# Optimization experiments

Measured on AMD Instinct MI355X. Metric: run time of the kernel, lower is better.

## Reference

```python
import jax, jax.numpy as jnp
import numpy as np

N_NODES, N_FEAT, HIDDEN, N_CLASSES, N_EDGES = 100000, 64, 64, 16, 1600000


def setup_inputs() -> dict:
    key = jax.random.key(0)
    ks = jax.random.split(key, 10)
    x = jax.random.normal(ks[0], (N_NODES, N_FEAT), dtype=jnp.float32)
    edge_index = jax.random.randint(ks[1], (2, N_EDGES), 0, N_NODES, dtype=jnp.int32)
    edge_weight = jax.random.uniform(ks[2], (N_EDGES,), dtype=jnp.float32)
    # Glorot-style init for GCNConv weights, zero bias (as in torch_geometric)
    W1 = jax.random.normal(ks[3], (N_FEAT, HIDDEN), dtype=jnp.float32) / np.float32(np.sqrt(N_FEAT))
    b1 = jnp.zeros((HIDDEN,), jnp.float32)
    W2 = jax.random.normal(ks[4], (HIDDEN, HIDDEN), dtype=jnp.float32) / np.float32(np.sqrt(HIDDEN))
    b2 = jnp.zeros((HIDDEN,), jnp.float32)
    W3 = jax.random.normal(ks[5], (HIDDEN, N_CLASSES), dtype=jnp.float32) / np.float32(np.sqrt(HIDDEN))
    b3 = jnp.zeros((N_CLASSES,), jnp.float32)
    return {"x": x, "edge_index": edge_index, "edge_weight": edge_weight,
            "W1": W1, "b1": b1, "W2": W2, "b2": b2, "W3": W3, "b3": b3}


def _gcn_norm(edge_index, edge_weight, num_nodes):
    """Add self-loops (weight 1) and compute symmetric D^-1/2 A D^-1/2 norm."""
    loop = jnp.arange(num_nodes, dtype=edge_index.dtype)
    src = jnp.concatenate([edge_index[0], loop])
    dst = jnp.concatenate([edge_index[1], loop])
    ew = jnp.concatenate([edge_weight, jnp.ones((num_nodes,), edge_weight.dtype)])
    deg = jax.ops.segment_sum(ew, dst, num_segments=num_nodes)
    dis = jnp.where(deg > 0, jax.lax.rsqrt(jnp.where(deg > 0, deg, 1.0)), 0.0)
    norm = dis[src] * ew * dis[dst]  # [E+N]
    return src, dst, norm


def reference(x, edge_index, edge_weight, W1, b1, W2, b2, W3, b3):
    N = x.shape[0]
    src, dst, norm = _gcn_norm(edge_index, edge_weight, N)

    def conv(h, W, b):
        hw = h @ W                                   # [N, out]
        msg = norm[:, None] * hw[src]                # [E+N, out]
        return jax.ops.segment_sum(msg, dst, num_segments=N) + b

    # conv1 + ReLU (dropout is identity in eval mode)
    h = jax.nn.relu(conv(x, W1, b1))
    # one hidden GCNConv layer (num_layer=3)
    h = jax.nn.relu(conv(h, W2, b2))
    logits = conv(h, W3, b3)                         # [N, C]
    out = jax.nn.log_softmax(logits, axis=1)
    return (out, logits, logits)
```

## Files before the change

kernel.cpp:

```cpp
#include <hip/hip_runtime.h>
#include <hip/hip_bf16.h>

#define N_FEAT 64
#define NBW 9
#define SRC_BITS 23
#define CAP 9216

typedef unsigned short u16;
typedef __attribute__((ext_vector_type(8))) short short8;
typedef __attribute__((ext_vector_type(4))) float f32x4;

__device__ inline u16 f2bf(float f) {
    unsigned u = __float_as_uint(f);
    u += 0x7fffu + ((u >> 16) & 1u);
    return (u16)(u >> 16);
}


__device__ inline void packW(const float* __restrict__ W, uint4* __restrict__ Wpk,
                             int ncb, int wcols, int tid) {
    int nf = ncb * 2 * 64;
    for (int f = tid; f < nf; f += 256) {
        int cb = f >> 7;
        int s  = (f >> 6) & 1;
        int lane = f & 63;
        int kb = lane >> 4, c16 = lane & 15;
        union { uint4 q; u16 u[8]; } pk;
        #pragma unroll
        for (int i = 0; i < 8; ++i) {
            int k = s * 32 + kb * 8 + i;
            pk.u[i] = f2bf(W[k * wcols + cb * 16 + c16]);
        }
        Wpk[f] = pk.q;
    }
}

__global__ __launch_bounds__(256) void pack_init(const float* __restrict__ W1, const float* __restrict__ W2,
                                                 const float* __restrict__ W3,
                                                 uint4* Wp1, uint4* Wp2, uint4* Wp3, int* bcur) {
    if (blockIdx.x == 0)      packW(W1, Wp1, 4, 64, threadIdx.x);
    else if (blockIdx.x == 1) packW(W2, Wp2, 4, 64, threadIdx.x);
    else if (blockIdx.x == 2) packW(W3, Wp3, 1, 16, threadIdx.x);
    else                      bcur[threadIdx.x] = 0;
}


template<int OUTW, bool INBF, bool SCALE>
__device__ inline void gemm_body(const void* __restrict__ Av, const uint4* __restrict__ Wpk,
                                 const float* __restrict__ dis, u16* __restrict__ C, int N,
                                 int wid, int lane) {
    constexpr int NCB = OUTW / 16;
    int r0 = wid * 16;
    if (r0 >= N) return;
    int row16 = lane & 15, kb = lane >> 4;
    int r = min(r0 + row16, N - 1);

    short8 a0, a1;
    if (INBF) {
        const u16* arow = (const u16*)Av + (size_t)r * 64 + kb * 8;
        a0 = __builtin_bit_cast(short8, *(const uint4*)arow);
        a1 = __builtin_bit_cast(short8, *(const uint4*)(arow + 32));
    } else {
        const float* arow = (const float*)Av + (size_t)r * 64 + kb * 8;
        float4 f0 = *(const float4*)arow;
        float4 f1 = *(const float4*)(arow + 4);
        float4 f2 = *(const float4*)(arow + 32);
        float4 f3 = *(const float4*)(arow + 36);
        union { short8 v; u16 u[8]; } pa, pb;
        pa.u[0] = f2bf(f0.x); pa.u[1] = f2bf(f0.y); pa.u[2] = f2bf(f0.z); pa.u[3] = f2bf(f0.w);
        pa.u[4] = f2bf(f1.x); pa.u[5] = f2bf(f1.y); pa.u[6] = f2bf(f1.z); pa.u[7] = f2bf(f1.w);
        pb.u[0] = f2bf(f2.x); pb.u[1] = f2bf(f2.y); pb.u[2] = f2bf(f2.z); pb.u[3] = f2bf(f2.w);
        pb.u[4] = f2bf(f3.x); pb.u[5] = f2bf(f3.y); pb.u[6] = f2bf(f3.z); pb.u[7] = f2bf(f3.w);
        a0 = pa.v; a1 = pb.v;
    }

    f32x4 acc[NCB];
    #pragma unroll
    for (int cb = 0; cb < NCB; ++cb) {
        short8 b0 = __builtin_bit_cast(short8, Wpk[(cb * 2 + 0) * 64 + lane]);
        short8 b1 = __builtin_bit_cast(short8, Wpk[(cb * 2 + 1) * 64 + lane]);
        f32x4 z = {0.f, 0.f, 0.f, 0.f};
        z = __builtin_amdgcn_mfma_f32_16x16x32_bf16(a0, b0, z, 0, 0, 0);
        z = __builtin_amdgcn_mfma_f32_16x16x32_bf16(a1, b1, z, 0, 0, 0);
        acc[cb] = z;
    }

    int rbase = r0 + kb * 4;
    float dsc[4];
    #pragma unroll
    for (int j = 0; j < 4; ++j) dsc[j] = SCALE ? dis[min(rbase + j, N - 1)] : 1.0f;

    #pragma unroll
    for (int cb = 0; cb < NCB; ++cb) {
        int col = cb * 16 + row16;
        #pragma unroll
        for (int j = 0; j < 4; ++j) {
            int rr = rbase + j;
            if (rr < N) C[(size_t)rr * OUTW + col] = f2bf(SCALE ? acc[cb][j] * dsc[j] : acc[cb][j]);
        }
    }
}


__global__ __launch_bounds__(256) void part_gemm(const int* __restrict__ ei, const float* __restrict__ ew,
                                                 int* bcur, int2* __restrict__ ebuf, int E, int NB, int PB,
                                                 const float* __restrict__ x, const uint4* __restrict__ Wp1,
                                                 u16* __restrict__ hwB, int N) {
    constexpr int EPT = 8;
    __shared__ int cnt[256];
    __shared__ int base[256];
    int tid = threadIdx.x;

    if ((int)blockIdx.x >= PB) {
        int wid = (int)(((blockIdx.x - PB) * blockDim.x + tid) >> 6);
        gemm_body<64, false, false>(x, Wp1, nullptr, hwB, N, wid, tid & 63);
        return;
    }

    cnt[tid] = 0;
    __syncthreads();
    int start = blockIdx.x * (256 * EPT);

    int d[EPT], r[EPT], s[EPT]; float w[EPT];
    #pragma unroll
    for (int i = 0; i < EPT; ++i) {
        int e = start + i * 256 + tid;
        if (e < E) {
            d[i] = ei[E + e];
            s[i] = ei[e];
            w[i] = ew[e];
            r[i] = atomicAdd(&cnt[d[i] >> NBW], 1);
        } else d[i] = -1;
    }
    __syncthreads();
    if (tid < NB && cnt[tid]) base[tid] = atomicAdd(&bcur[tid], cnt[tid]);
    __syncthreads();
    #pragma unroll
    for (int i = 0; i < EPT; ++i) {
        if (d[i] >= 0) {
            int b = d[i] >> NBW;
            int dl = d[i] & ((1 << NBW) - 1);
            int gpos = base[b] + r[i];
            if (gpos < CAP) {
                int key = (dl << SRC_BITS) | s[i];
                ebuf[(size_t)b * CAP + gpos] = make_int2(key, __float_as_int(w[i]));
            }
        }
    }
}

__global__ __launch_bounds__(256) void bucket_csr(const int2* __restrict__ ebuf, const int* __restrict__ bcur,
                                                  int2* __restrict__ csr, int* __restrict__ rowp,
                                                  int* __restrict__ cnt, float* __restrict__ dis, int N) {
    __shared__ int   h[512];
    __shared__ float ws[512];
    __shared__ int   off[512];
    __shared__ int   wsum[4];
    int b = blockIdx.x, tid = threadIdx.x;
    int nbase = b << NBW;
    int nn = min(512, N - nbase);
    int beg = b * CAP;
    int m = min(bcur[b], CAP);

    h[tid] = 0; h[tid + 256] = 0;
    ws[tid] = 0.f; ws[tid + 256] = 0.f;
    __syncthreads();

    for (int i = tid; i < m; i += 256) {
        int2 en = ebuf[beg + i];
        int dl = ((unsigned)en.x) >> SRC_BITS;
        atomicAdd(&h[dl], 1);
        atomicAdd(&ws[dl], __int_as_float(en.y));
    }
    __syncthreads();

    int v0 = h[2 * tid], v1 = h[2 * tid + 1];
    int v = v0 + v1;
    int lane = tid & 63, wv = tid >> 6;
    int incl = v;
    #pragma unroll
    for (int o = 1; o < 64; o <<= 1) { int t = __shfl_up(incl, o); if (lane >= o) incl += t; }
    if (lane == 63) wsum[wv] = incl;
    __syncthreads();
    int add = 0;
    #pragma unroll
    for (int i = 0; i < 4; ++i) if (i < wv) add += wsum[i];
    int excl = add + incl - v;
    off[2 * tid] = excl;
    off[2 * tid + 1] = excl + v0;
    __syncthreads();

    for (int l = tid; l < nn; l += 256) {
        rowp[nbase + l] = beg + off[l];
        cnt[nbase + l]  = h[l];
        dis[nbase + l]  = rsqrtf(1.0f + ws[l]);
    }
    __syncthreads();
    h[tid] = 0; h[tid + 256] = 0;
    __syncthreads();

    for (int i = tid; i < m; i += 256) {
        int2 en = ebuf[beg + i];
        unsigned k = (unsigned)en.x;
        int dl  = k >> SRC_BITS;
        int src = k & ((1 << SRC_BITS) - 1);
        int pos = atomicAdd(&h[dl], 1);
        csr[beg + off[dl] + pos] = make_int2(src, en.y);
    }
}


template<int OUTW, bool LOADDIS>
__global__ __launch_bounds__(256) void agg_gemm(const u16* __restrict__ hw, const int* __restrict__ rowp,
                                                const int* __restrict__ cnt, const int2* __restrict__ csr,
                                                const float* __restrict__ dis, const float* __restrict__ bias,
                                                const uint4* __restrict__ Wpk, u16* __restrict__ C, int N) {
    constexpr int UN = 8;
    __shared__ u16 As[32 * 64];

    int tid  = threadIdx.x;
    int w    = tid >> 6;
    int lane = tid & 63;
    int g = lane >> 3;
    int t = lane & 7;
    int l = w * 8 + g;
    int n = blockIdx.x * 32 + l;
    bool alive = (n < N);
    n = min(n, N - 1);

    float dd = dis[n];
    int beg = rowp[n];
    int c   = cnt[n];
    const char* hwb = (const char*)hw;
    unsigned toff = (unsigned)t * 16u;

    float acc[8];
    {
        uint4 raw = *(const uint4*)(hwb + (unsigned)n * 128u + toff);
        float sw = LOADDIS ? dd : 1.0f;
        unsigned uw[4] = {raw.x, raw.y, raw.z, raw.w};
        #pragma unroll
        for (int k = 0; k < 4; ++k) {
            acc[2 * k]     = sw * __uint_as_float(uw[k] << 16);
            acc[2 * k + 1] = sw * __uint_as_float(uw[k] & 0xffff0000u);
        }
    }

    for (int j0 = 0; j0 < c; j0 += UN) {
        int2 e[UN];
        #pragma unroll
        for (int i = 0; i < UN; ++i) e[i] = csr[beg + min(j0 + i, c - 1)];
        uint4 r[UN]; float wgt[UN];
        #pragma unroll
        for (int i = 0; i < UN; ++i) {
            r[i] = *(const uint4*)(hwb + (unsigned)e[i].x * 128u + toff);
            float wr = __int_as_float(e[i].y);
            if (LOADDIS) wr *= dis[e[i].x];
            wgt[i] = (j0 + i < c) ? wr : 0.0f;
        }
        #pragma unroll
        for (int i = 0; i < UN; ++i) {
            unsigned u[4] = {r[i].x, r[i].y, r[i].z, r[i].w};
            #pragma unroll
            for (int k = 0; k < 4; ++k) {
                acc[2 * k]     = fmaf(wgt[i], __uint_as_float(u[k] << 16), acc[2 * k]);
                acc[2 * k + 1] = fmaf(wgt[i], __uint_as_float(u[k] & 0xffff0000u), acc[2 * k + 1]);
            }
        }
    }

    {
        float4 b0 = *(const float4*)&bias[t * 8];
        float4 b1 = *(const float4*)&bias[t * 8 + 4];
        float bb[8] = {b0.x, b0.y, b0.z, b0.w, b1.x, b1.y, b1.z, b1.w};
        #pragma unroll
        for (int k = 0; k < 8; ++k) acc[k] = fmaxf(fmaf(dd, acc[k], bb[k]), 0.0f);
        uint4 pk;
        pk.x = (unsigned)f2bf(acc[0]) | ((unsigned)f2bf(acc[1]) << 16);
        pk.y = (unsigned)f2bf(acc[2]) | ((unsigned)f2bf(acc[3]) << 16);
        pk.z = (unsigned)f2bf(acc[4]) | ((unsigned)f2bf(acc[5]) << 16);
        pk.w = (unsigned)f2bf(acc[6]) | ((unsigned)f2bf(acc[7]) << 16);
        *(uint4*)&As[l * 64 + t * 8] = pk;
    }
    __syncthreads();

    if (w < 2) {
        constexpr int NCB = OUTW / 16;
        int r0 = blockIdx.x * 32 + w * 16;
        if (r0 < N) {
            int row16 = lane & 15, kb = lane >> 4;
            const u16* arow = &As[(w * 16 + row16) * 64 + kb * 8];
            short8 a0 = __builtin_bit_cast(short8, *(const uint4*)arow);
            short8 a1 = __builtin_bit_cast(short8, *(const uint4*)(arow + 32));

            f32x4 za[NCB];
            #pragma unroll
            for (int cb = 0; cb < NCB; ++cb) {
                short8 b0 = __builtin_bit_cast(short8, Wpk[(cb * 2 + 0) * 64 + lane]);
                short8 b1 = __builtin_bit_cast(short8, Wpk[(cb * 2 + 1) * 64 + lane]);
                f32x4 z = {0.f, 0.f, 0.f, 0.f};
                z = __builtin_amdgcn_mfma_f32_16x16x32_bf16(a0, b0, z, 0, 0, 0);
                z = __builtin_amdgcn_mfma_f32_16x16x32_bf16(a1, b1, z, 0, 0, 0);
                za[cb] = z;
            }

            int rbase = r0 + kb * 4;
            float dsc[4];
            #pragma unroll
            for (int j = 0; j < 4; ++j) dsc[j] = dis[min(rbase + j, N - 1)];
            #pragma unroll
            for (int cb = 0; cb < NCB; ++cb) {
                int col = cb * 16 + row16;
                #pragma unroll
                for (int j = 0; j < 4; ++j) {
                    int rr = rbase + j;
                    if (rr < N) C[(size_t)rr * OUTW + col] = f2bf(za[cb][j] * dsc[j]);
                }
            }
        }
    }
}


__global__ __launch_bounds__(256) void agg_final(const u16* __restrict__ hw, const int* __restrict__ rowp,
                                                 const int* __restrict__ cnt, const int2* __restrict__ csr,
                                                 const float* __restrict__ dis, const float* __restrict__ bias,
                                                 float* __restrict__ out0, float* __restrict__ out2,
                                                 float* __restrict__ out3, int N) {
    constexpr int UN = 8;
    int wv   = (int)((blockIdx.x * blockDim.x + threadIdx.x) >> 6);
    int lane = threadIdx.x & 63;
    int g = lane >> 1;
    int t = lane & 1;
    int n = wv * 32 + g;
    bool alive = (n < N);
    n = min(n, N - 1);

    float dd = dis[n];
    int beg = rowp[n];
    int c   = cnt[n];
    const char* hwb = (const char*)hw;
    unsigned toff = (unsigned)t * 16u;

    float acc[8];
    {
        uint4 raw = *(const uint4*)(hwb + (unsigned)n * 32u + toff);
        unsigned uw[4] = {raw.x, raw.y, raw.z, raw.w};
        #pragma unroll
        for (int k = 0; k < 4; ++k) {
            acc[2 * k]     = __uint_as_float(uw[k] << 16);
            acc[2 * k + 1] = __uint_as_float(uw[k] & 0xffff0000u);
        }
    }

    for (int j0 = 0; j0 < c; j0 += UN) {
        int2 e[UN];
        #pragma unroll
        for (int i = 0; i < UN; ++i) e[i] = csr[beg + min(j0 + i, c - 1)];
        uint4 r[UN]; float wgt[UN];
        #pragma unroll
        for (int i = 0; i < UN; ++i) {
            r[i] = *(const uint4*)(hwb + (unsigned)e[i].x * 32u + toff);
            wgt[i] = (j0 + i < c) ? __int_as_float(e[i].y) : 0.0f;
        }
        #pragma unroll
        for (int i = 0; i < UN; ++i) {
            unsigned u[4] = {r[i].x, r[i].y, r[i].z, r[i].w};
            #pragma unroll
            for (int k = 0; k < 4; ++k) {
                acc[2 * k]     = fmaf(wgt[i], __uint_as_float(u[k] << 16), acc[2 * k]);
                acc[2 * k + 1] = fmaf(wgt[i], __uint_as_float(u[k] & 0xffff0000u), acc[2 * k + 1]);
            }
        }
    }

    if (alive) {
        float4 b0 = *(const float4*)&bias[t * 8];
        float4 b1 = *(const float4*)&bias[t * 8 + 4];
        float bb[8] = {b0.x, b0.y, b0.z, b0.w, b1.x, b1.y, b1.z, b1.w};
        #pragma unroll
        for (int k = 0; k < 8; ++k) acc[k] = fmaf(dd, acc[k], bb[k]);

        float4 r0 = make_float4(acc[0], acc[1], acc[2], acc[3]);
        float4 r1 = make_float4(acc[4], acc[5], acc[6], acc[7]);
        *(float4*)&out2[(size_t)n * 16 + t * 8] = r0;
        *(float4*)&out2[(size_t)n * 16 + t * 8 + 4] = r1;
        *(float4*)&out3[(size_t)n * 16 + t * 8] = r0;
        *(float4*)&out3[(size_t)n * 16 + t * 8 + 4] = r1;
        float mloc = acc[0];
        #pragma unroll
        for (int k = 1; k < 8; ++k) mloc = fmaxf(mloc, acc[k]);
        float m = fmaxf(mloc, __shfl_xor(mloc, 1));
        float sloc = 0.f;
        #pragma unroll
        for (int k = 0; k < 8; ++k) sloc += __expf(acc[k] - m);
        float ssum = sloc + __shfl_xor(sloc, 1);
        float ls = m + __logf(ssum);
        float4 w0 = make_float4(acc[0] - ls, acc[1] - ls, acc[2] - ls, acc[3] - ls);
        float4 w1 = make_float4(acc[4] - ls, acc[5] - ls, acc[6] - ls, acc[7] - ls);
        *(float4*)&out0[(size_t)n * 16 + t * 8] = w0;
        *(float4*)&out0[(size_t)n * 16 + t * 8 + 4] = w1;
    }
}


extern "C" void kernel_launch(void* const* d_in, const int* in_sizes, int n_in,
                              void* d_out, int out_size, void* d_ws, size_t ws_size,
                              hipStream_t stream) {
    const float* x   = (const float*)d_in[0];
    const int*   ei  = (const int*)d_in[1];
    const float* ew  = (const float*)d_in[2];
    const float* W1  = (const float*)d_in[3];
    const float* b1  = (const float*)d_in[4];
    const float* W2  = (const float*)d_in[5];
    const float* b2  = (const float*)d_in[6];
    const float* W3  = (const float*)d_in[7];
    const float* b3  = (const float*)d_in[8];
    float* out = (float*)d_out;

    const int N = in_sizes[0] / N_FEAT;
    const int E = in_sizes[2];
    const int NB = (N + (1 << NBW) - 1) >> NBW;

    size_t off = 0;
    auto alloc = [&](size_t bytes) {
        void* p = (char*)d_ws + off;
        off += (bytes + 255) & ~(size_t)255;
        return p;
    };
    float* dis     = (float*)alloc((size_t)N * 4);
    int*   cnt     = (int*)alloc((size_t)N * 4);
    int*   rowp    = (int*)alloc((size_t)N * 4);
    int*   bcur    = (int*)alloc(256 * 4);
    int2*  csr     = (int2*)alloc((size_t)NB * CAP * 8);
    int2*  ebuf    = (int2*)alloc((size_t)NB * CAP * 8);
    u16*   hwB     = (u16*)alloc((size_t)N * 64 * 2);
    u16*   hwB2    = (u16*)alloc((size_t)N * 64 * 2);
    u16*   hw16    = (u16*)alloc((size_t)N * 16 * 2);
    uint4* Wp1     = (uint4*)alloc(512 * 16);
    uint4* Wp2     = (uint4*)alloc(512 * 16);
    uint4* Wp3     = (uint4*)alloc(128 * 16);

    const int TB = 256;

    int gblk = ((N + 15) / 16 + 3) / 4;
    int PB   = (E + 2047) / 2048;
    int fblk = (N + 31) / 32;
    int ablk16 = (N * 2 + TB - 1) / TB;

    float* logits = out + (size_t)N * 16;
    float* logits2 = out + (size_t)2 * N * 16;

    pack_init<<<4, TB, 0, stream>>>(W1, W2, W3, Wp1, Wp2, Wp3, bcur);
    part_gemm<<<PB + gblk, TB, 0, stream>>>(ei, ew, bcur, ebuf, E, NB, PB, x, Wp1, hwB, N);
    bucket_csr<<<NB, TB, 0, stream>>>(ebuf, bcur, csr, rowp, cnt, dis, N);

    agg_gemm<64, true><<<fblk, TB, 0, stream>>>(hwB, rowp, cnt, csr, dis, b1, Wp2, hwB2, N);
    agg_gemm<16, false><<<fblk, TB, 0, stream>>>(hwB2, rowp, cnt, csr, dis, b2, Wp3, hw16, N);
    agg_final<<<ablk16, TB, 0, stream>>>(hw16, rowp, cnt, csr, dis, b3, out, logits, logits2, N);
}
```

Baseline: 168.3 us.

## Software-prefetch CSR edges in aggregation loops and split MFMA epilogue across four waves

The aggregation loops in agg_gemm and agg_final now prefetch the next batch of CSR edge entries while the current gathers are in flight. This removes the dependent index-load latency from each iteration. To allow unclamped over-reads, the CSR buffer is padded and 16 zero entries are written after each bucket. For OUTW=64, the MFMA epilogue is split across all four waves, each computing two column blocks, instead of two waves computing four. This trades extra registers and a larger buffer for more overlap.

```diff
diff --git a/kernel.cpp b/kernel.cpp
--- a/kernel.cpp
+++ b/kernel.cpp
@@ -207,6 +207,8 @@
         int pos = atomicAdd(&h[dl], 1);
         csr[beg + off[dl] + pos] = make_int2(src, en.y);
     }
+
+    if (tid < 16) csr[beg + m + tid] = make_int2(0, 0);
 }
 
 
@@ -225,7 +227,6 @@
     int t = lane & 7;
     int l = w * 8 + g;
     int n = blockIdx.x * 32 + l;
-    bool alive = (n < N);
     n = min(n, N - 1);
 
     float dd = dis[n];
@@ -246,14 +247,20 @@
         }
     }
 
+    int2 e[UN];
+    #pragma unroll
+    for (int i = 0; i < UN; ++i) e[i] = csr[beg + i];
     for (int j0 = 0; j0 < c; j0 += UN) {
-        int2 e[UN];
-        #pragma unroll
-        for (int i = 0; i < UN; ++i) e[i] = csr[beg + min(j0 + i, c - 1)];
-        uint4 r[UN]; float wgt[UN];
+        uint4 r[UN];
+        #pragma unroll
+        for (int i = 0; i < UN; ++i)
+            r[i] = *(const uint4*)(hwb + (unsigned)e[i].x * 128u + toff);
+        int2 en[UN];
+        #pragma unroll
+        for (int i = 0; i < UN; ++i) en[i] = csr[beg + j0 + UN + i];
+        float wgt[UN];
         #pragma unroll
         for (int i = 0; i < UN; ++i) {
-            r[i] = *(const uint4*)(hwb + (unsigned)e[i].x * 128u + toff);
             float wr = __int_as_float(e[i].y);
             if (LOADDIS) wr *= dis[e[i].x];
             wgt[i] = (j0 + i < c) ? wr : 0.0f;
@@ -267,6 +274,8 @@
                 acc[2 * k + 1] = fmaf(wgt[i], __uint_as_float(u[k] & 0xffff0000u), acc[2 * k + 1]);
             }
         }
+        #pragma unroll
+        for (int i = 0; i < UN; ++i) e[i] = en[i];
     }
 
     {
@@ -284,24 +293,25 @@
     }
     __syncthreads();
 
-    if (w < 2) {
-        constexpr int NCB = OUTW / 16;
-        int r0 = blockIdx.x * 32 + w * 16;
+    if (OUTW == 64) {
+        int tile = w >> 1, half = w & 1;
+        int r0 = blockIdx.x * 32 + tile * 16;
         if (r0 < N) {
             int row16 = lane & 15, kb = lane >> 4;
-            const u16* arow = &As[(w * 16 + row16) * 64 + kb * 8];
+            const u16* arow = &As[(tile * 16 + row16) * 64 + kb * 8];
             short8 a0 = __builtin_bit_cast(short8, *(const uint4*)arow);
             short8 a1 = __builtin_bit_cast(short8, *(const uint4*)(arow + 32));
 
-            f32x4 za[NCB];
+            f32x4 za[2];
             #pragma unroll
-            for (int cb = 0; cb < NCB; ++cb) {
+            for (int c2 = 0; c2 < 2; ++c2) {
+                int cb = half * 2 + c2;
                 short8 b0 = __builtin_bit_cast(short8, Wpk[(cb * 2 + 0) * 64 + lane]);
                 short8 b1 = __builtin_bit_cast(short8, Wpk[(cb * 2 + 1) * 64 + lane]);
                 f32x4 z = {0.f, 0.f, 0.f, 0.f};
                 z = __builtin_amdgcn_mfma_f32_16x16x32_bf16(a0, b0, z, 0, 0, 0);
                 z = __builtin_amdgcn_mfma_f32_16x16x32_bf16(a1, b1, z, 0, 0, 0);
-                za[cb] = z;
+                za[c2] = z;
             }
 
             int rbase = r0 + kb * 4;
@@ -309,12 +319,38 @@
             #pragma unroll
             for (int j = 0; j < 4; ++j) dsc[j] = dis[min(rbase + j, N - 1)];
             #pragma unroll
-            for (int cb = 0; cb < NCB; ++cb) {
-                int col = cb * 16 + row16;
+            for (int c2 = 0; c2 < 2; ++c2) {
+                int col = (half * 2 + c2) * 16 + row16;
                 #pragma unroll
                 for (int j = 0; j < 4; ++j) {
                     int rr = rbase + j;
-                    if (rr < N) C[(size_t)rr * OUTW + col] = f2bf(za[cb][j] * dsc[j]);
+                    if (rr < N) C[(size_t)rr * 64 + col] = f2bf(za[c2][j] * dsc[j]);
+                }
+            }
+        }
+    } else {
+        if (w < 2) {
+            int r0 = blockIdx.x * 32 + w * 16;
+            if (r0 < N) {
+                int row16 = lane & 15, kb = lane >> 4;
+                const u16* arow = &As[(w * 16 + row16) * 64 + kb * 8];
+                short8 a0 = __builtin_bit_cast(short8, *(const uint4*)arow);
+                short8 a1 = __builtin_bit_cast(short8, *(const uint4*)(arow + 32));
+                short8 b0 = __builtin_bit_cast(short8, Wpk[0 * 64 + lane]);
+                short8 b1 = __builtin_bit_cast(short8, Wpk[1 * 64 + lane]);
+                f32x4 z = {0.f, 0.f, 0.f, 0.f};
+                z = __builtin_amdgcn_mfma_f32_16x16x32_bf16(a0, b0, z, 0, 0, 0);
+                z = __builtin_amdgcn_mfma_f32_16x16x32_bf16(a1, b1, z, 0, 0, 0);
+
+                int rbase = r0 + kb * 4;
+                float dsc[4];
+                #pragma unroll
+                for (int j = 0; j < 4; ++j) dsc[j] = dis[min(rbase + j, N - 1)];
+                int col = row16;
+                #pragma unroll
+                for (int j = 0; j < 4; ++j) {
+                    int rr = rbase + j;
+                    if (rr < N) C[(size_t)rr * 16 + col] = f2bf(z[j] * dsc[j]);
                 }
             }
         }
@@ -353,16 +389,20 @@
         }
     }
 
+    int2 e[UN];
+    #pragma unroll
+    for (int i = 0; i < UN; ++i) e[i] = csr[beg + i];
     for (int j0 = 0; j0 < c; j0 += UN) {
-        int2 e[UN];
-        #pragma unroll
-        for (int i = 0; i < UN; ++i) e[i] = csr[beg + min(j0 + i, c - 1)];
-        uint4 r[UN]; float wgt[UN];
-        #pragma unroll
-        for (int i = 0; i < UN; ++i) {
+        uint4 r[UN];
+        #pragma unroll
+        for (int i = 0; i < UN; ++i)
             r[i] = *(const uint4*)(hwb + (unsigned)e[i].x * 32u + toff);
-            wgt[i] = (j0 + i < c) ? __int_as_float(e[i].y) : 0.0f;
-        }
+        int2 en[UN];
+        #pragma unroll
+        for (int i = 0; i < UN; ++i) en[i] = csr[beg + j0 + UN + i];
+        float wgt[UN];
+        #pragma unroll
+        for (int i = 0; i < UN; ++i) wgt[i] = (j0 + i < c) ? __int_as_float(e[i].y) : 0.0f;
         #pragma unroll
         for (int i = 0; i < UN; ++i) {
             unsigned u[4] = {r[i].x, r[i].y, r[i].z, r[i].w};
@@ -372,6 +412,8 @@
                 acc[2 * k + 1] = fmaf(wgt[i], __uint_as_float(u[k] & 0xffff0000u), acc[2 * k + 1]);
             }
         }
+        #pragma unroll
+        for (int i = 0; i < UN; ++i) e[i] = en[i];
     }
 
     if (alive) {
@@ -432,7 +474,7 @@
     int*   cnt     = (int*)alloc((size_t)N * 4);
     int*   rowp    = (int*)alloc((size_t)N * 4);
     int*   bcur    = (int*)alloc(256 * 4);
-    int2*  csr     = (int2*)alloc((size_t)NB * CAP * 8);
+    int2*  csr     = (int2*)alloc(((size_t)NB * CAP + 32) * 8);
     int2*  ebuf    = (int2*)alloc((size_t)NB * CAP * 8);
     u16*   hwB     = (u16*)alloc((size_t)N * 64 * 2);
     u16*   hwB2    = (u16*)alloc((size_t)N * 64 * 2);
```

After: 163.8 us. -2.7%, faster.
